# Kernel optimization log

Hardware: AMD Instinct MI355X
Metric: run time of the kernel (lower is better)

## Reference

```python
import jax, jax.numpy as jnp
import numpy as np

EPS = 1e-5


def _binary_act(x):
    # Forward: sign(x). Backward: piecewise-polynomial surrogate (ApproxSign STE).
    out3 = jnp.where(x < -1, -1.0,
            jnp.where(x < 0, x * x + 2.0 * x,
             jnp.where(x < 1, -x * x + 2.0 * x, 1.0)))
    return jax.lax.stop_gradient(jnp.sign(x) - out3) + out3


def _binarize_weights(w):
    # Per-output-channel scaling factor (detached), forward = scale*sign(w),
    # backward flows through clamp(w, -1, 1) (STE).
    scale = jax.lax.stop_gradient(jnp.mean(jnp.abs(w), axis=(1, 2, 3), keepdims=True))
    clipped = jnp.clip(w, -1.0, 1.0)
    return jax.lax.stop_gradient(scale * jnp.sign(w) - clipped) + clipped


def setup_inputs() -> dict:
    key = jax.random.key(0)
    kx, kw = jax.random.split(key)
    B, Cin, Cout, H, W = 32, 128, 128, 56, 56
    x = jax.random.normal(kx, (B, Cin, H, W), dtype=jnp.float32)
    # HardBinaryConv: weight = rand(n)*0.001 permuted then reshaped -> just random in [0, 0.001)
    w = jax.random.uniform(kw, (Cout, Cin, 3, 3), dtype=jnp.float32) * 0.001
    return {
        "x": x,
        "bias0": jnp.zeros((Cin,), jnp.float32),   # move0 LearnableBias
        "w": w,                                     # HardBinaryConv latent weights
        "gamma": jnp.ones((Cout,), jnp.float32),    # BN weight
        "beta": jnp.zeros((Cout,), jnp.float32),    # BN bias
        "bias1": jnp.zeros((Cout,), jnp.float32),   # move1
        "alpha": jnp.full((Cout,), 0.25, jnp.float32),  # PReLU per-channel
        "bias2": jnp.zeros((Cout,), jnp.float32),   # move2
    }


def reference(x, bias0, w, gamma, beta, bias1, alpha, bias2):
    def pc(v):  # per-channel broadcast (1, C, 1, 1)
        return v[None, :, None, None]

    residual = x
    out = x + pc(bias0)                     # move0
    out = _binary_act(out)                  # binary activation
    bw = _binarize_weights(w)               # {-scale, +scale} weights
    y = jax.lax.conv_general_dilated(
        out, bw, window_strides=(1, 1), padding=((1, 1), (1, 1)),
        dimension_numbers=("NCHW", "OIHW", "NCHW"))
    # BatchNorm2d (training mode: biased batch statistics over N,H,W)
    mean = jnp.mean(y, axis=(0, 2, 3), keepdims=True)
    var = jnp.mean(jnp.square(y - mean), axis=(0, 2, 3), keepdims=True)
    y = (y - mean) * jax.lax.rsqrt(var + EPS) * pc(gamma) + pc(beta)
    y = y + residual
    y = y + pc(bias1)                       # move1
    y = jnp.where(y >= 0, y, pc(alpha) * y)  # PReLU
    y = y + pc(bias2)                       # move2
    return y
```

## Files before the change

### kernel.cpp

```cpp
#include <hip/hip_runtime.h>
#include <stdint.h>

#define NB 32
#define NC 128
#define NH 56
#define NW 56
#define NHW_ (NH * NW)
#define NPIX (NB * NHW_)
#define NO 128
#define NK 1152
#define NRP 28
#define NSLOT (NB * NRP)

#define PADH 58
#define PADW 66
#define PAD_BYTES ((size_t)NB * PADH * PADW * 2 * 8)

typedef unsigned long long u64;

__global__ __launch_bounds__(256) void pack_act(const float* __restrict__ x,
                                                const float* __restrict__ bias0,
                                                u64* __restrict__ packAp) {
    int p = blockIdx.x * 256 + threadIdx.x;
    if (p >= NPIX) return;
    int n = p / NHW_;
    int rem = p - n * NHW_;
    int h = rem / NW, wcol = rem - h * NW;
    const float* xb = x + (size_t)n * NC * NHW_ + rem;
    u64 w0 = 0, w1 = 0;
#pragma unroll 8
    for (int c = 0; c < 64; ++c)
        w0 |= (u64)((xb[(size_t)c * NHW_] + bias0[c]) > 0.f) << c;
#pragma unroll 8
    for (int c = 0; c < 64; ++c)
        w1 |= (u64)((xb[(size_t)(c + 64) * NHW_] + bias0[c + 64]) > 0.f) << c;
    size_t idx = (((size_t)n * PADH + (h + 1)) * PADW + (wcol + 1)) * 2;
    packAp[idx]     = w0;
    packAp[idx + 1] = w1;
}

__global__ __launch_bounds__(64) void pack_wgt(const float* __restrict__ w,
                                               u64* __restrict__ packW,
                                               float* __restrict__ scaleW,
                                               int* __restrict__ corrW) {
    __shared__ u64 sb[18];
    int o = blockIdx.x;
    int t = threadIdx.x;
    const float* wo = w + (size_t)o * NK;
    float s = 0.f;
    for (int i = t; i < NK; i += 64) s += fabsf(wo[i]);
    for (int off = 32; off; off >>= 1) s += __shfl_down(s, off);
    if (t == 0) scaleW[o] = s / (float)NK;
    if (t < 18) {
        int tap = t >> 1;
        int j   = t & 1;
        u64 bits = 0;
        for (int cc = 0; cc < 64; ++cc) {
            int c = j * 64 + cc;
            bits |= (u64)(wo[c * 9 + tap] > 0.f) << cc;
        }
        packW[(size_t)o * 18 + t] = bits;
        sb[t] = bits;
    }
    __syncthreads();
    if (t == 0) {
        int cv[9];
#pragma unroll
        for (int tap = 0; tap < 9; ++tap)
            cv[tap] = NC - 2 * (__popcll(sb[2 * tap]) + __popcll(sb[2 * tap + 1]));
        int* cw = corrW + o * 8;
        cw[0] = cv[0] + cv[3] + cv[6];
        cw[1] = cv[2] + cv[5] + cv[8];
        cw[2] = cv[0] + cv[1] + cv[2];
        cw[3] = cv[6] + cv[7] + cv[8];
        cw[4] = cv[0];
        cw[5] = cv[2];
        cw[6] = cv[6];
        cw[7] = cv[8];
    }
}

template <int MODE>
__global__ __launch_bounds__(256) void conv_bin(
    const u64* __restrict__ packAp, const u64* __restrict__ packW,
    const int* __restrict__ corrW, short* __restrict__ yI,
    int* __restrict__ sumP, int* __restrict__ sqP,
    const float* __restrict__ coefA, const float* __restrict__ coefB,
    const float* __restrict__ alpha, const float* __restrict__ bias2,
    const float* __restrict__ x, float* __restrict__ out) {
    int bid = blockIdx.x;
    int n = bid / (NRP * 2);
    int rem = bid - n * (NRP * 2);
    int hp = rem >> 1;
    int cg = rem & 1;
    int h0 = hp * 2;

    int wv = threadIdx.x >> 6, lane = threadIdx.x & 63;
    bool act = lane < NW;

    u64 a[4][3][2];
    const u64* bp = packAp + (((size_t)n * PADH + h0) * PADW + lane) * 2;
#pragma unroll
    for (int r = 0; r < 4; ++r)
#pragma unroll
        for (int c = 0; c < 3; ++c) {
            ulonglong2 q = *reinterpret_cast<const ulonglong2*>(
                bp + ((size_t)r * PADW + c) * 2);
            a[r][c][0] = q.x;
            a[r][c][1] = q.y;
        }

    int obase = __builtin_amdgcn_readfirstlane(cg * 64 + (wv << 4));
    const u64* wbase = packW + (size_t)obase * 18;
    const int* cbase = corrW + obase * 8;

    bool top = (hp == 0), bot = (hp == NRP - 1);
    bool isL = (lane == 0), isR = (lane == NW - 1);
    int sl = n * NRP + hp;
    size_t pixoff = (size_t)n * NO * NHW_ + (size_t)h0 * NW + lane;

    for (int oo = 0; oo < 16; ++oo) {
        int o = obase + oo;
        const u64* wp = wbase + oo * 18;
        const int* cw = cbase + oo * 8;
        int pc0 = 0, pc1 = 0;
#pragma unroll
        for (int t = 0; t < 9; ++t) {
            const int kh = t / 3, kw = t - 3 * (t / 3);
            u64 w0 = wp[2 * t], w1 = wp[2 * t + 1];
            pc0 += __popcll(a[kh][kw][0] ^ w0) + __popcll(a[kh][kw][1] ^ w1);
            pc1 += __popcll(a[kh + 1][kw][0] ^ w0) + __popcll(a[kh + 1][kw][1] ^ w1);
        }
        int corrcol = isL ? cw[0] : (isR ? cw[1] : 0);
        int base = NK - corrcol;
        int d0 = base - 2 * pc0;
        int d1 = base - 2 * pc1;
        if (top) d0 -= cw[2] - (isL ? cw[4] : (isR ? cw[5] : 0));
        if (bot) d1 -= cw[3] - (isL ? cw[6] : (isR ? cw[7] : 0));

        if (MODE == 0 && act) {
            short* yp = yI + pixoff + (size_t)o * NHW_;
            yp[0]  = (short)d0;
            yp[NW] = (short)d1;
        }
        if (MODE <= 1) {
            int s = act ? (d0 + d1) : 0;
            int q = act ? (__mul24(d0, d0) + __mul24(d1, d1)) : 0;
#pragma unroll
            for (int off = 32; off; off >>= 1) {
                s += __shfl_down(s, off);
                q += __shfl_down(q, off);
            }
            if (lane == 0) {
                sumP[o * NSLOT + sl] = s;
                sqP[o * NSLOT + sl]  = q;
            }
        }
        if (MODE == 2 && act) {
            float ca = coefA[o], cb = coefB[o], al = alpha[o], b2 = bias2[o];
            size_t idx = pixoff + (size_t)o * NHW_;
            float t0 = fmaf(ca, (float)d0, cb) + x[idx];
            float t1 = fmaf(ca, (float)d1, cb) + x[idx + NW];
            t0 = t0 >= 0.f ? t0 : al * t0;
            t1 = t1 >= 0.f ? t1 : al * t1;
            out[idx]      = t0 + b2;
            out[idx + NW] = t1 + b2;
        }
    }
}

__global__ __launch_bounds__(64) void bn_coef2(const int* __restrict__ sumP,
                                               const int* __restrict__ sqP,
                                               const float* __restrict__ scaleW,
                                               const float* __restrict__ gamma,
                                               const float* __restrict__ beta,
                                               const float* __restrict__ bias1,
                                               float* __restrict__ coefA,
                                               float* __restrict__ coefB) {
    int o = blockIdx.x;
    int t = threadIdx.x;
    long long s = 0, q = 0;
    for (int i = t; i < NSLOT; i += 64) {
        s += sumP[o * NSLOT + i];
        q += sqP[o * NSLOT + i];
    }
#pragma unroll
    for (int off = 32; off; off >>= 1) {
        s += __shfl_down(s, off);
        q += __shfl_down(q, off);
    }
    if (t == 0) {
        double cnt = (double)NPIX;
        double mean = (double)s / cnt;
        double var = (double)q / cnt - mean * mean;
        if (var < 0.0) var = 0.0;
        float sc = scaleW[o];
        float rs = rsqrtf((float)((double)sc * (double)sc * var) + 1e-5f);
        float g = gamma[o];
        coefA[o] = sc * g * rs;
        coefB[o] = beta[o] - (float)((double)sc * mean) * g * rs + bias1[o];
    }
}

__global__ __launch_bounds__(256) void final_store(const short* __restrict__ yI,
                                                   const float* __restrict__ x,
                                                   const float* __restrict__ coefA,
                                                   const float* __restrict__ coefB,
                                                   const float* __restrict__ alpha,
                                                   const float* __restrict__ bias2,
                                                   float* __restrict__ out) {
    const size_t ngroups = (size_t)NB * NO * NHW_ / 8;
    for (size_t g = (size_t)blockIdx.x * blockDim.x + threadIdx.x; g < ngroups;
         g += (size_t)gridDim.x * blockDim.x) {
        size_t i = g * 8;
        int o = (int)((i / NHW_) % NO);
        float a = coefA[o], bb = coefB[o], al = alpha[o], b2 = bias2[o];
        int4 yv = *reinterpret_cast<const int4*>(yI + i);
        float4 x0 = *reinterpret_cast<const float4*>(x + i);
        float4 x1 = *reinterpret_cast<const float4*>(x + i + 4);
        int q[4] = {yv.x, yv.y, yv.z, yv.w};
        float xs[8] = {x0.x, x0.y, x0.z, x0.w, x1.x, x1.y, x1.z, x1.w};
        float r[8];
#pragma unroll
        for (int j = 0; j < 4; ++j) {
            float lo = (float)(short)(q[j] & 0xffff);
            float hi = (float)(q[j] >> 16);
            float t0 = fmaf(a, lo, bb) + xs[2 * j];
            float t1 = fmaf(a, hi, bb) + xs[2 * j + 1];
            t0 = t0 >= 0.f ? t0 : al * t0;
            t1 = t1 >= 0.f ? t1 : al * t1;
            r[2 * j]     = t0 + b2;
            r[2 * j + 1] = t1 + b2;
        }
        float4 o0 = {r[0], r[1], r[2], r[3]};
        float4 o1 = {r[4], r[5], r[6], r[7]};
        *reinterpret_cast<float4*>(out + i)     = o0;
        *reinterpret_cast<float4*>(out + i + 4) = o1;
    }
}

extern "C" void kernel_launch(void* const* d_in, const int* in_sizes, int n_in,
                              void* d_out, int out_size, void* d_ws, size_t ws_size,
                              hipStream_t stream) {
    (void)in_sizes; (void)n_in; (void)out_size;
    const float* x     = (const float*)d_in[0];
    const float* bias0 = (const float*)d_in[1];
    const float* w     = (const float*)d_in[2];
    const float* gamma = (const float*)d_in[3];
    const float* beta  = (const float*)d_in[4];
    const float* bias1 = (const float*)d_in[5];
    const float* alpha = (const float*)d_in[6];
    const float* bias2 = (const float*)d_in[7];
    float* out = (float*)d_out;
    char* ws = (char*)d_ws;

    u64*   packAp = (u64*)ws;
    u64*   packW  = (u64*)(ws + 1959936);
    int*   corrW  = (int*)(ws + 1978368);
    float* scaleW = (float*)(ws + 1982464);
    float* coefA  = (float*)(ws + 1982976);
    float* coefB  = (float*)(ws + 1983488);
    int*   sumP   = (int*)(ws + 1984000);
    int*   sqP    = (int*)(ws + 2442752);
    short* yI     = (short*)(ws + 2901504);
    bool store = ws_size >= (size_t)2901504 + (size_t)NB * NO * NHW_ * 2;

    hipMemsetAsync(packAp, 0, PAD_BYTES, stream);
    pack_act<<<NPIX / 256, 256, 0, stream>>>(x, bias0, packAp);
    pack_wgt<<<NO, 64, 0, stream>>>(w, packW, scaleW, corrW);

    if (store) {
        conv_bin<0><<<NB * NRP * 2, 256, 0, stream>>>(
            packAp, packW, corrW, yI, sumP, sqP,
            nullptr, nullptr, nullptr, nullptr, nullptr, nullptr);
        bn_coef2<<<NO, 64, 0, stream>>>(sumP, sqP, scaleW, gamma, beta, bias1, coefA, coefB);
        final_store<<<2048, 256, 0, stream>>>(yI, x, coefA, coefB, alpha, bias2, out);
    } else {
        conv_bin<1><<<NB * NRP * 2, 256, 0, stream>>>(
            packAp, packW, corrW, nullptr, sumP, sqP,
            nullptr, nullptr, nullptr, nullptr, nullptr, nullptr);
        bn_coef2<<<NO, 64, 0, stream>>>(sumP, sqP, scaleW, gamma, beta, bias1, coefA, coefB);
        conv_bin<2><<<NB * NRP * 2, 256, 0, stream>>>(
            packAp, packW, corrW, nullptr, sumP, sqP,
            coefA, coefB, alpha, bias2, x, out);
    }
}
```

Baseline: 100.3 us.

## Transpose packed weights tap-major and reorder conv loop to tap-outer

Packed binary weights are now stored tap-major ([tap][out channel][2]), so each wave reads 16 consecutive channels' words for one tap as one contiguous scalar block. The conv loop is inverted: for each kernel column it loads 4 activation rows, then accumulates popcounts for all 16 output channels into register arrays. The 12-entry activation register tile is replaced by a 4-row slice, which lowers its footprint and may allow wider scalar loads. The cost is 32 accumulators held in registers, which raises register pressure and could affect occupancy.

```diff
diff --git a/kernel.cpp b/kernel.cpp
--- a/kernel.cpp
+++ b/kernel.cpp
@@ -40,7 +40,7 @@
 }
 
 __global__ __launch_bounds__(64) void pack_wgt(const float* __restrict__ w,
-                                               u64* __restrict__ packW,
+                                               u64* __restrict__ packWT,
                                                float* __restrict__ scaleW,
                                                int* __restrict__ corrW) {
     __shared__ u64 sb[18];
@@ -59,7 +59,7 @@
             int c = j * 64 + cc;
             bits |= (u64)(wo[c * 9 + tap] > 0.f) << cc;
         }
-        packW[(size_t)o * 18 + t] = bits;
+        packWT[((size_t)tap * NO + o) * 2 + j] = bits;
         sb[t] = bits;
     }
     __syncthreads();
@@ -82,7 +82,7 @@
 
 template <int MODE>
 __global__ __launch_bounds__(256) void conv_bin(
-    const u64* __restrict__ packAp, const u64* __restrict__ packW,
+    const u64* __restrict__ packAp, const u64* __restrict__ packWT,
     const int* __restrict__ corrW, short* __restrict__ yI,
     int* __restrict__ sumP, int* __restrict__ sqP,
     const float* __restrict__ coefA, const float* __restrict__ coefB,
@@ -97,44 +97,50 @@
 
     int wv = threadIdx.x >> 6, lane = threadIdx.x & 63;
     bool act = lane < NW;
-
-    u64 a[4][3][2];
+    int obase = __builtin_amdgcn_readfirstlane(cg * 64 + (wv << 4));
+
     const u64* bp = packAp + (((size_t)n * PADH + h0) * PADW + lane) * 2;
-#pragma unroll
-    for (int r = 0; r < 4; ++r)
-#pragma unroll
-        for (int c = 0; c < 3; ++c) {
+
+    int pc0[16], pc1[16];
+#pragma unroll
+    for (int i = 0; i < 16; ++i) { pc0[i] = 0; pc1[i] = 0; }
+
+#pragma unroll
+    for (int kw = 0; kw < 3; ++kw) {
+        u64 A[4][2];
+#pragma unroll
+        for (int r = 0; r < 4; ++r) {
             ulonglong2 q = *reinterpret_cast<const ulonglong2*>(
-                bp + ((size_t)r * PADW + c) * 2);
-            a[r][c][0] = q.x;
-            a[r][c][1] = q.y;
-        }
-
-    int obase = __builtin_amdgcn_readfirstlane(cg * 64 + (wv << 4));
-    const u64* wbase = packW + (size_t)obase * 18;
-    const int* cbase = corrW + obase * 8;
+                bp + ((size_t)r * PADW + kw) * 2);
+            A[r][0] = q.x;
+            A[r][1] = q.y;
+        }
+#pragma unroll
+        for (int kh = 0; kh < 3; ++kh) {
+            const u64* wt = packWT + ((size_t)(kh * 3 + kw) * NO + obase) * 2;
+#pragma unroll
+            for (int ch = 0; ch < 16; ++ch) {
+                u64 w0 = wt[2 * ch], w1 = wt[2 * ch + 1];
+                pc0[ch] += __popcll(A[kh][0] ^ w0) + __popcll(A[kh][1] ^ w1);
+                pc1[ch] += __popcll(A[kh + 1][0] ^ w0) + __popcll(A[kh + 1][1] ^ w1);
+            }
+        }
+    }
 
     bool top = (hp == 0), bot = (hp == NRP - 1);
     bool isL = (lane == 0), isR = (lane == NW - 1);
     int sl = n * NRP + hp;
     size_t pixoff = (size_t)n * NO * NHW_ + (size_t)h0 * NW + lane;
-
-    for (int oo = 0; oo < 16; ++oo) {
-        int o = obase + oo;
-        const u64* wp = wbase + oo * 18;
-        const int* cw = cbase + oo * 8;
-        int pc0 = 0, pc1 = 0;
-#pragma unroll
-        for (int t = 0; t < 9; ++t) {
-            const int kh = t / 3, kw = t - 3 * (t / 3);
-            u64 w0 = wp[2 * t], w1 = wp[2 * t + 1];
-            pc0 += __popcll(a[kh][kw][0] ^ w0) + __popcll(a[kh][kw][1] ^ w1);
-            pc1 += __popcll(a[kh + 1][kw][0] ^ w0) + __popcll(a[kh + 1][kw][1] ^ w1);
-        }
+    const int* cbase = corrW + obase * 8;
+
+#pragma unroll
+    for (int ch = 0; ch < 16; ++ch) {
+        int o = obase + ch;
+        const int* cw = cbase + ch * 8;
         int corrcol = isL ? cw[0] : (isR ? cw[1] : 0);
         int base = NK - corrcol;
-        int d0 = base - 2 * pc0;
-        int d1 = base - 2 * pc1;
+        int d0 = base - 2 * pc0[ch];
+        int d1 = base - 2 * pc1[ch];
         if (top) d0 -= cw[2] - (isL ? cw[4] : (isR ? cw[5] : 0));
         if (bot) d1 -= cw[3] - (isL ? cw[6] : (isR ? cw[7] : 0));
 
@@ -255,7 +261,7 @@
     char* ws = (char*)d_ws;
 
     u64*   packAp = (u64*)ws;
-    u64*   packW  = (u64*)(ws + 1959936);
+    u64*   packWT = (u64*)(ws + 1959936);
     int*   corrW  = (int*)(ws + 1978368);
     float* scaleW = (float*)(ws + 1982464);
     float* coefA  = (float*)(ws + 1982976);
@@ -267,21 +273,21 @@
 
     hipMemsetAsync(packAp, 0, PAD_BYTES, stream);
     pack_act<<<NPIX / 256, 256, 0, stream>>>(x, bias0, packAp);
-    pack_wgt<<<NO, 64, 0, stream>>>(w, packW, scaleW, corrW);
+    pack_wgt<<<NO, 64, 0, stream>>>(w, packWT, scaleW, corrW);
 
     if (store) {
         conv_bin<0><<<NB * NRP * 2, 256, 0, stream>>>(
-            packAp, packW, corrW, yI, sumP, sqP,
+            packAp, packWT, corrW, yI, sumP, sqP,
             nullptr, nullptr, nullptr, nullptr, nullptr, nullptr);
         bn_coef2<<<NO, 64, 0, stream>>>(sumP, sqP, scaleW, gamma, beta, bias1, coefA, coefB);
         final_store<<<2048, 256, 0, stream>>>(yI, x, coefA, coefB, alpha, bias2, out);
     } else {
         conv_bin<1><<<NB * NRP * 2, 256, 0, stream>>>(
-            packAp, packW, corrW, nullptr, sumP, sqP,
+            packAp, packWT, corrW, nullptr, sumP, sqP,
             nullptr, nullptr, nullptr, nullptr, nullptr, nullptr);
         bn_coef2<<<NO, 64, 0, stream>>>(sumP, sqP, scaleW, gamma, beta, bias1, coefA, coefB);
         conv_bin<2><<<NB * NRP * 2, 256, 0, stream>>>(
-            packAp, packW, corrW, nullptr, sumP, sqP,
+            packAp, packWT, corrW, nullptr, sumP, sqP,
             coefA, coefB, alpha, bias2, x, out);
     }
 }
```

New measurement: 156.1 us. +55.6%, slower.
